# Kernel tuning notes

Measured on AMD Instinct MI355X. Metric: run time of the kernel, lower is better.

Reference implementation:

```python
import jax, jax.numpy as jnp
import numpy as np

B, L, N, F, H, ED, HOR = 64, 24, 512, 2, 128, 16, 12


def setup_inputs() -> dict:
    key = jax.random.key(0)
    ks = jax.random.split(key, 9)
    g = lambda k, shp, sc: jax.random.normal(k, shp, dtype=jnp.float32) * sc
    return {
        "X": g(ks[0], (B, L, N, F), 1.0),
        "E": g(ks[1], (N, ED), 1.0),
        "W1": g(ks[2], (ED, ED), ED ** -0.5),
        "W2": g(ks[3], (ED, ED), ED ** -0.5),
        "Wz": g(ks[4], (F + H, H), (F + H) ** -0.5),
        "bz": jnp.zeros((H,), jnp.float32),
        "Wr": g(ks[5], (F + H, H), (F + H) ** -0.5),
        "br": jnp.zeros((H,), jnp.float32),
        "Wh": g(ks[6], (F + H, H), (F + H) ** -0.5),
        "bh": jnp.zeros((H,), jnp.float32),
        "Whead": g(ks[7], (H, HOR), H ** -0.5),
        "bhead": jnp.zeros((HOR,), jnp.float32),
    }


def reference(X, E, W1, W2, Wz, bz, Wr, br, Wh, bh, Whead, bhead):
    # Adaptive adjacency: A = softmax(relu((E W1)(E W2)^T))  -> [N, N]
    M1 = E @ W1
    M2 = E @ W2
    A = jax.nn.softmax(jax.nn.relu(M1 @ M2.T), axis=-1)

    b, n, h = X.shape[0], X.shape[2], Wz.shape[1]

    def step(hprev, x_t):  # x_t: [B, N, F], hprev: [B, N, H]
        inp = jnp.concatenate([x_t, hprev], axis=-1)          # [B, N, F+H]
        g = jnp.einsum('nm,bmf->bnf', A, inp)                  # graph conv mix
        z = jax.nn.sigmoid(g @ Wz + bz)
        r = jax.nn.sigmoid(g @ Wr + br)
        inp_r = jnp.concatenate([x_t, r * hprev], axis=-1)
        gh = jnp.einsum('nm,bmf->bnf', A, inp_r)
        h_tilde = jnp.tanh(gh @ Wh + bh)
        hnew = (1.0 - z) * hprev + z * h_tilde
        return hnew, None

    h0 = jnp.zeros((b, n, h), X.dtype)
    h_final, _ = jax.lax.scan(step, h0, jnp.moveaxis(X, 1, 0))  # scan over L
    out = h_final @ Whead + bhead                                # [B, N, HOR]
    return jnp.transpose(out, (0, 2, 1))                         # [B, HOR, N]
```

## Files before the change

### kernel.cpp

```cpp
#include <hip/hip_runtime.h>

typedef _Float16 f16;
typedef _Float16 f16x8 __attribute__((ext_vector_type(8)));
typedef float f32x4 __attribute__((ext_vector_type(4)));

typedef const __attribute__((address_space(1))) void GV;
typedef __attribute__((address_space(3))) void LV;

__device__ __forceinline__ void gload16(const void* g, void* l) {
  __builtin_amdgcn_global_load_lds((GV*)g, (LV*)l, 16, 0, 0);
}

#define WAIT_VM0() asm volatile("s_waitcnt vmcnt(0)" ::: "memory")

__device__ __forceinline__ f16x8 ntload16(const f16* p) {
  f16x8 v;
  asm volatile("global_load_dwordx4 %0, %1, off sc0 sc1" : "=v"(v) : "v"(p) : "memory");
  return v;
}
__device__ __forceinline__ void ntstore16(f16* p, f16x8 v) {
  asm volatile("global_store_dwordx4 %0, %1, off sc0 sc1" :: "v"(p), "v"(v) : "memory");
}

__device__ __forceinline__ void group_sync(unsigned* bar, unsigned target) {
  __syncthreads();
  if (threadIdx.x == 0) {
    atomicAdd(bar, 1u);
    int guard = 0;
    while (1) {
      unsigned v;
      asm volatile("global_load_dword %0, %1, off sc0 sc1\n\ts_waitcnt vmcnt(0)"
                   : "=v"(v) : "v"(bar) : "memory");
      if (v >= target || ++guard > (1 << 22)) break;
      __builtin_amdgcn_s_sleep(8);
    }
  }
  __syncthreads();
}

__device__ __forceinline__ f16x8 frag64(const f16* T, int row, int chunk) {
  int ch = chunk ^ (row & 7);
  return *(const f16x8*)((const char*)T + row * 128 + ch * 16);
}
__device__ __forceinline__ f16x8 frag128(const f16* T, int row, int chunk) {
  int ch = chunk ^ (row & 15);
  return *(const f16x8*)((const char*)T + row * 256 + ch * 16);
}
__device__ __forceinline__ f16* elem128(f16* T, int row, int col) {
  return (f16*)((char*)T + row * 256 + (((col >> 3) ^ (row & 15)) << 4) + (col & 7) * 2);
}

#define MFMA(a, b, c) __builtin_amdgcn_mfma_f32_16x16x32_f16(a, b, c, 0, 0, 0)

__device__ __forceinline__ float sigm(float v) {
  return __builtin_amdgcn_rcpf(1.f + __expf(-v));
}
__device__ __forceinline__ float tanh_(float v) {
  return 1.f - 2.f * __builtin_amdgcn_rcpf(1.f + __expf(2.f * v));
}

__device__ __forceinline__ void issue64(const f16* Ab, const f16* Bb, int k0,
                                        char* bufA, f16x8 (&c)[4],
                                        const size_t (&offs)[4], int wb) {
#pragma unroll
  for (int q = 0; q < 4; ++q)
    gload16(Ab + k0 + offs[q], bufA + q * 4096 + wb);
#pragma unroll
  for (int q = 0; q < 4; ++q)
    c[q] = ntload16(Bb + k0 + offs[q]);
}
__device__ __forceinline__ void wr64(char* bufB, const f16x8 (&c)[4], int tb) {
#pragma unroll
  for (int q = 0; q < 4; ++q)
    *(f16x8*)(bufB + q * 4096 + tb) = c[q];
}
__device__ __forceinline__ void comp64(const char* buf, int wm, int wn, int g, int r,
                                       f32x4 (&acc)[4][4]) {
  const f16* Ta = (const f16*)buf;
  const f16* Tb = (const f16*)(buf + 16384);
#pragma unroll
  for (int kk = 0; kk < 2; ++kk) {
    f16x8 af[4], bf[4];
#pragma unroll
    for (int i = 0; i < 4; ++i) af[i] = frag64(Ta, wm + i * 16 + r, (kk << 2) | g);
#pragma unroll
    for (int j = 0; j < 4; ++j) bf[j] = frag64(Tb, wn + j * 16 + r, (kk << 2) | g);
#pragma unroll
    for (int i = 0; i < 4; ++i)
#pragma unroll
      for (int j = 0; j < 4; ++j)
        acc[i][j] = MFMA(af[i], bf[j], acc[i][j]);
  }
}

__device__ __forceinline__ void phase1(const f16* At, const f16* Bb, char* sm,
    const size_t (&offs)[4], int wm, int wn, int g, int r, f32x4 (&acc)[4][4]) {
  const int tid = threadIdx.x;
  const int wb = (tid >> 6) * 1024;
  const int tb = tid * 16;
  f16x8 c[4];
  issue64(At, Bb, 0, sm, c, offs, wb);
  WAIT_VM0();
  wr64(sm + 16384, c, tb);
  __syncthreads();
#pragma unroll 1
  for (int kt = 0; kt < 8; ++kt) {
    char* cur = sm + (kt & 1) * 32768;
    char* nxt = sm + ((kt & 1) ^ 1) * 32768;
    if (kt < 7) issue64(At, Bb, (kt + 1) * 64, nxt, c, offs, wb);
    comp64(cur, wm, wn, g, r, acc);
    if (kt < 7) { WAIT_VM0(); wr64(nxt + 16384, c, tb); }
    __syncthreads();
  }
}

__device__ __forceinline__ void gate_gemm(const f16* Gs, const f16* WT,
                                          int wm, int wn, int g, int r,
                                          f32x4 (&acc)[4][4]) {
#pragma unroll
  for (int kk = 0; kk < 4; ++kk) {
    f16x8 wf[4], af[4];
#pragma unroll
    for (int j = 0; j < 4; ++j)
      wf[j] = *(const f16x8*)&WT[(size_t)(wn + j * 16 + r) * 128 + kk * 32 + g * 8];
#pragma unroll
    for (int i = 0; i < 4; ++i) af[i] = frag128(Gs, wm + i * 16 + r, (kk << 2) | g);
#pragma unroll
    for (int i = 0; i < 4; ++i)
#pragma unroll
      for (int j = 0; j < 4; ++j)
        acc[i][j] = MFMA(af[i], wf[j], acc[i][j]);
  }
}

__global__ __launch_bounds__(256, 1)
void persist(const f16* __restrict__ A16, const f16* __restrict__ AX,
             const f16* __restrict__ WzT, const f16* __restrict__ WrT,
             const f16* __restrict__ WhT,
             const float* __restrict__ Wzf, const float* __restrict__ bz,
             const float* __restrict__ Wrf, const float* __restrict__ br,
             const float* __restrict__ Whf, const float* __restrict__ bh,
             const float* __restrict__ Whead, const float* __restrict__ bhead,
             f16* __restrict__ Ha, f16* __restrict__ Hb,
             f16* __restrict__ RH, unsigned* __restrict__ bar,
             float* __restrict__ out) {
  __shared__ __align__(16) char sm[136192];
  f16* Gs = (f16*)(sm + 65536);
  f16* Ct = (f16*)(sm + 98304);
  f16* AXs = (f16*)(sm + 131072);
  float* wp = (float*)(sm + 131584);

  const int tid = threadIdx.x;
  const int lane = tid & 63;
  const int g = lane >> 4, r = lane & 15;
  const int wid = tid >> 6;
  const int wm = (wid >> 1) * 64, wn = (wid & 1) * 64;
  const int b = blockIdx.x >> 2, nc = blockIdx.x & 3;
  const int m0 = nc * 128;

  for (int idx = tid; idx < 1152; idx += 256) {
    int row = idx >> 7, j = idx & 127;
    float v;
    if (row == 0) v = Wzf[j];
    else if (row == 1) v = Wzf[128 + j];
    else if (row == 2) v = bz[j];
    else if (row == 3) v = Wrf[j];
    else if (row == 4) v = Wrf[128 + j];
    else if (row == 5) v = br[j];
    else if (row == 6) v = Whf[j];
    else if (row == 7) v = Whf[128 + j];
    else v = bh[j];
    wp[idx] = v;
  }

  size_t offs[4];
#pragma unroll
  for (int q = 0; q < 4; ++q) {
    int lin = q * 4096 + tid * 16;
    int row = lin >> 7;
    int ch = ((lin >> 4) & 7) ^ (row & 7);
    offs[q] = (size_t)row * 512 + ch * 8;
  }

  const f16* Atile = A16 + (size_t)m0 * 512;
  const size_t boff = (size_t)b * 65536;
  f16* rh = RH + boff;
  unsigned* mybar = bar + b * 16;
  unsigned nbar = 0;
  f16x8 zreg[8];
  f16x8 hvreg[8] = {};

#pragma unroll 1
  for (int t = 0; t < 24; ++t) {
    const f16* hc = ((t & 1) ? Hb : Ha) + boff;
    f16* hn = ((t & 1) ? Ha : Hb) + boff;
    if (tid < 128) {
      int cf = b * 48 + t * 2;
      const f16* p = AX + (size_t)(cf >> 7) * 65536 + (size_t)(m0 + tid) * 128 + (cf & 127);
      AXs[2 * tid] = p[0];
      AXs[2 * tid + 1] = p[1];
    }
    f32x4 acc[4][4] = {};
    phase1(Atile, hc, sm, offs, wm, wn, g, r, acc);
#pragma unroll
    for (int i = 0; i < 4; ++i)
#pragma unroll
      for (int j = 0; j < 4; ++j)
#pragma unroll
        for (int q = 0; q < 4; ++q)
          *elem128(Gs, wm + i * 16 + g * 4 + q, wn + j * 16 + r) = (f16)acc[i][j][q];
    __syncthreads();
    {
      f32x4 az[4][4] = {};
      gate_gemm(Gs, WzT, wm, wn, g, r, az);
#pragma unroll
      for (int i = 0; i < 4; ++i)
#pragma unroll
        for (int j = 0; j < 4; ++j)
#pragma unroll
          for (int q = 0; q < 4; ++q)
            *elem128(Ct, wn + j * 16 + r, wm + i * 16 + g * 4 + q) = (f16)az[i][j][q];
      __syncthreads();
#pragma unroll
      for (int p = 0; p < 8; ++p) {
        int hh = p * 16 + (tid >> 4), c = tid & 15, nl0 = c * 8;
        f16x8 cv = frag128(Ct, hh, c);
        float w0 = wp[hh], w1 = wp[128 + hh], bb = wp[256 + hh];
        f16x8 o;
#pragma unroll
        for (int e = 0; e < 8; ++e) {
          int nl = nl0 + e;
          float gx = (float)AXs[2 * nl] * w0 + (float)AXs[2 * nl + 1] * w1 + bb;
          o[e] = (f16)sigm((float)cv[e] + gx);
        }
        zreg[p] = o;
      }
      __syncthreads();
    }
    {
      f32x4 ar[4][4] = {};
      gate_gemm(Gs, WrT, wm, wn, g, r, ar);
#pragma unroll
      for (int i = 0; i < 4; ++i)
#pragma unroll
        for (int j = 0; j < 4; ++j)
#pragma unroll
          for (int q = 0; q < 4; ++q)
            *elem128(Ct, wn + j * 16 + r, wm + i * 16 + g * 4 + q) = (f16)ar[i][j][q];
      __syncthreads();
#pragma unroll
      for (int p = 0; p < 8; ++p) {
        int hh = p * 16 + (tid >> 4), c = tid & 15, nl0 = c * 8;
        f16x8 cv = frag128(Ct, hh, c);
        f16x8 hv = hvreg[p];
        float w0 = wp[384 + hh], w1 = wp[512 + hh], bb = wp[640 + hh];
        f16x8 o;
#pragma unroll
        for (int e = 0; e < 8; ++e) {
          int nl = nl0 + e;
          float gx = (float)AXs[2 * nl] * w0 + (float)AXs[2 * nl + 1] * w1 + bb;
          float rv = sigm((float)cv[e] + gx);
          o[e] = (f16)(rv * (float)hv[e]);
        }
        ntstore16(&rh[(size_t)hh * 512 + m0 + nl0], o);
      }
    }
    group_sync(mybar, 4u * (++nbar));
    f32x4 acc2[4][4] = {};
    phase1(Atile, rh, sm, offs, wm, wn, g, r, acc2);
#pragma unroll
    for (int i = 0; i < 4; ++i)
#pragma unroll
      for (int j = 0; j < 4; ++j)
#pragma unroll
        for (int q = 0; q < 4; ++q)
          *elem128(Gs, wm + i * 16 + g * 4 + q, wn + j * 16 + r) = (f16)acc2[i][j][q];
    __syncthreads();
    {
      f32x4 ah[4][4] = {};
      gate_gemm(Gs, WhT, wm, wn, g, r, ah);
#pragma unroll
      for (int i = 0; i < 4; ++i)
#pragma unroll
        for (int j = 0; j < 4; ++j)
#pragma unroll
          for (int q = 0; q < 4; ++q)
            *elem128(Ct, wn + j * 16 + r, wm + i * 16 + g * 4 + q) = (f16)ah[i][j][q];
      __syncthreads();
#pragma unroll
      for (int p = 0; p < 8; ++p) {
        int hh = p * 16 + (tid >> 4), c = tid & 15, nl0 = c * 8;
        f16x8 cv = frag128(Ct, hh, c);
        float w0 = wp[768 + hh], w1 = wp[896 + hh], bb = wp[1024 + hh];
        f16x8 hv = hvreg[p], zv = zreg[p];
        f16x8 o;
#pragma unroll
        for (int e = 0; e < 8; ++e) {
          int nl = nl0 + e;
          float gx = (float)AXs[2 * nl] * w0 + (float)AXs[2 * nl + 1] * w1 + bb;
          float ht = tanh_((float)cv[e] + gx);
          float z = (float)zv[e];
          o[e] = (f16)((1.f - z) * (float)hv[e] + z * ht);
        }
        hvreg[p] = o;
        if (t < 23) {
          ntstore16(&hn[(size_t)hh * 512 + m0 + nl0], o);
        } else {
          *(f16x8*)((char*)Gs + hh * 256 + nl0 * 2) = o;
        }
      }
    }
    if (t < 23) {
      group_sync(mybar, 4u * (++nbar));
    }
  }

  __syncthreads();
  float* Ws = (float*)Ct;
  for (int idx = tid; idx < 1548; idx += 256)
    Ws[idx] = (idx < 1536) ? Whead[idx] : bhead[idx - 1536];
  __syncthreads();
  {
    int n = tid & 127, half = tid >> 7;
    float pa[12];
#pragma unroll
    for (int o = 0; o < 12; ++o) pa[o] = 0.f;
    const f16* Hfin = (const f16*)Gs;
    for (int h = half * 64; h < half * 64 + 64; ++h) {
      float v = (float)Hfin[h * 128 + n];
#pragma unroll
      for (int o = 0; o < 12; ++o) pa[o] = fmaf(v, Ws[h * 12 + o], pa[o]);
    }
    float* P = (float*)(sm + 40960);
#pragma unroll
    for (int o = 0; o < 12; ++o) P[(n * 2 + half) * 12 + o] = pa[o];
    __syncthreads();
    if (half == 0) {
#pragma unroll
      for (int o = 0; o < 12; ++o)
        out[(size_t)b * 6144 + o * 512 + m0 + n] = P[n * 24 + o] + P[n * 24 + 12 + o] + Ws[1536 + o];
    }
  }
}

__device__ __forceinline__ void stage128x64(const f16* src, int row0, int ld, int k0,
                                            f16* lds, int tid) {
  int wid = tid >> 6;
#pragma unroll
  for (int q = 0; q < 4; ++q) {
    int lin = q * 4096 + tid * 16;
    int row = lin >> 7;
    int ch = (lin >> 4) & 7;
    int sch = ch ^ (row & 7);
    gload16(src + (size_t)(row0 + row) * ld + k0 + sch * 8,
            (char*)lds + q * 4096 + wid * 1024);
  }
}

__global__ __launch_bounds__(256, 2)
void gemm512(const f16* __restrict__ A, const f16* __restrict__ B,
             f16* __restrict__ C) {
  __shared__ __align__(16) char sm[34816];
  f16* As = (f16*)sm;
  f16* Bs = (f16*)(sm + 16384);
  const int tid = threadIdx.x;
  const int lane = tid & 63;
  const int g = lane >> 4, r = lane & 15;
  const int wid = tid >> 6;
  const int wm = (wid >> 1) * 64, wn = (wid & 1) * 64;
  const int m0 = blockIdx.y * 128;
  const int n0 = blockIdx.x * 128;
  f32x4 acc[4][4] = {};
  for (int kt = 0; kt < 8; ++kt) {
    stage128x64(A, m0, 512, kt * 64, As, tid);
    stage128x64(B, n0, 512, kt * 64, Bs, tid);
    __syncthreads();
#pragma unroll
    for (int kk = 0; kk < 2; ++kk) {
      f16x8 af[4], bf[4];
#pragma unroll
      for (int i = 0; i < 4; ++i) af[i] = frag64(As, wm + i * 16 + r, (kk << 2) | g);
#pragma unroll
      for (int j = 0; j < 4; ++j) bf[j] = frag64(Bs, wn + j * 16 + r, (kk << 2) | g);
#pragma unroll
      for (int i = 0; i < 4; ++i)
#pragma unroll
        for (int j = 0; j < 4; ++j)
          acc[i][j] = MFMA(af[i], bf[j], acc[i][j]);
    }
    __syncthreads();
  }
  f16* Ctl = (f16*)sm;
#pragma unroll
  for (int i = 0; i < 4; ++i)
#pragma unroll
    for (int j = 0; j < 4; ++j) {
      int col = wn + j * 16 + r;
#pragma unroll
      for (int q = 0; q < 4; ++q) {
        int row = wm + i * 16 + g * 4 + q;
        Ctl[row * 136 + col] = (f16)acc[i][j][q];
      }
    }
  __syncthreads();
  f16* Cb = C + (size_t)blockIdx.x * 65536;
#pragma unroll
  for (int p = 0; p < 8; ++p) {
    int row = p * 16 + (tid >> 4);
    int c0 = (tid & 15) * 8;
    f16x8 v = *(const f16x8*)&Ctl[row * 136 + c0];
    *(f16x8*)&Cb[(size_t)(m0 + row) * 128 + c0] = v;
  }
}

__global__ void m12k(const float* __restrict__ E, const float* __restrict__ W1,
                     const float* __restrict__ W2, float* __restrict__ M1,
                     float* __restrict__ M2) {
  int idx = blockIdx.x * 256 + threadIdx.x;
  if (idx >= 16384) return;
  int which = idx >> 13;
  int rem = idx & 8191;
  int n = rem >> 4, j = rem & 15;
  const float* W = which ? W2 : W1;
  float s = 0.f;
#pragma unroll
  for (int k = 0; k < 16; ++k) s += E[n * 16 + k] * W[k * 16 + j];
  (which ? M2 : M1)[n * 16 + j] = s;
}

__global__ __launch_bounds__(256)
void softA(const float* __restrict__ M1, const float* __restrict__ M2,
           f16* __restrict__ A16) {
  __shared__ float M2s[8192];
  __shared__ float m1s[16];
  __shared__ float red[8];
  int i = blockIdx.x, tid = threadIdx.x;
  for (int q = tid; q < 8192; q += 256) M2s[q] = M2[q];
  if (tid < 16) m1s[tid] = M1[i * 16 + tid];
  __syncthreads();
  float s0 = 0.f, s1 = 0.f;
#pragma unroll
  for (int k = 0; k < 16; ++k) {
    float a = m1s[k];
    s0 += a * M2s[tid * 16 + k];
    s1 += a * M2s[(tid + 256) * 16 + k];
  }
  s0 = fmaxf(s0, 0.f);
  s1 = fmaxf(s1, 0.f);
  float m = fmaxf(s0, s1);
  for (int o = 32; o > 0; o >>= 1) m = fmaxf(m, __shfl_xor(m, o));
  if ((tid & 63) == 0) red[tid >> 6] = m;
  __syncthreads();
  m = fmaxf(fmaxf(red[0], red[1]), fmaxf(red[2], red[3]));
  float e0 = expf(s0 - m), e1 = expf(s1 - m);
  float ss = e0 + e1;
  for (int o = 32; o > 0; o >>= 1) ss += __shfl_xor(ss, o);
  __syncthreads();
  if ((tid & 63) == 0) red[4 + (tid >> 6)] = ss;
  __syncthreads();
  ss = (red[4] + red[5]) + (red[6] + red[7]);
  float inv = 1.f / ss;
  A16[(size_t)i * 512 + tid] = (f16)(e0 * inv);
  A16[(size_t)i * 512 + tid + 256] = (f16)(e1 * inv);
}

__global__ void wTk(const float* __restrict__ Wz, const float* __restrict__ Wr,
                    const float* __restrict__ Wh, f16* __restrict__ WzT,
                    f16* __restrict__ WrT, f16* __restrict__ WhT) {
  int idx = blockIdx.x * 256 + threadIdx.x;
  if (idx >= 49152) return;
  int w = idx / 16384;
  int rem = idx & 16383;
  int hp = rem >> 7, k = rem & 127;
  const float* S = (w == 0) ? Wz : ((w == 1) ? Wr : Wh);
  f16* D = (w == 0) ? WzT : ((w == 1) ? WrT : WhT);
  D[hp * 128 + k] = (f16)S[(2 + k) * 128 + hp];
}

__global__ void xTk(const float* __restrict__ X, f16* __restrict__ XTT) {
  int idx = blockIdx.x * 256 + threadIdx.x;
  if (idx >= 786432) return;
  int m = idx & 511;
  int bt = idx >> 9;
  float x0 = X[(size_t)idx * 2];
  float x1 = X[(size_t)idx * 2 + 1];
  XTT[(size_t)(bt * 2 + 0) * 512 + m] = (f16)x0;
  XTT[(size_t)(bt * 2 + 1) * 512 + m] = (f16)x1;
}

extern "C" void kernel_launch(void* const* d_in, const int* in_sizes, int n_in,
                              void* d_out, int out_size, void* d_ws, size_t ws_size,
                              hipStream_t stream) {
  (void)in_sizes; (void)n_in; (void)out_size; (void)ws_size;
  const float* X = (const float*)d_in[0];
  const float* E = (const float*)d_in[1];
  const float* W1 = (const float*)d_in[2];
  const float* W2 = (const float*)d_in[3];
  const float* Wz = (const float*)d_in[4];
  const float* bz = (const float*)d_in[5];
  const float* Wr = (const float*)d_in[6];
  const float* br = (const float*)d_in[7];
  const float* Wh = (const float*)d_in[8];
  const float* bh = (const float*)d_in[9];
  const float* Whead = (const float*)d_in[10];
  const float* bhead = (const float*)d_in[11];
  float* out = (float*)d_out;
  char* ws = (char*)d_ws;

  f16* A16 = (f16*)(ws + 0);
  f16* XTT = (f16*)(ws + 524288);
  f16* AX  = (f16*)(ws + 3670016);
  f16* Ha  = (f16*)(ws + 6815744);
  f16* Hb  = (f16*)(ws + 15204352);
  f16* RH  = (f16*)(ws + 23592960);
  f16* WzT = (f16*)(ws + 31981568);
  f16* WrT = (f16*)(ws + 32014336);
  f16* WhT = (f16*)(ws + 32047104);
  float* M1 = (float*)(ws + 32079872);
  float* M2 = (float*)(ws + 32112640);
  unsigned* bar = (unsigned*)(ws + 32145408);

  hipMemsetAsync(Ha, 0, 8388608, stream);
  hipMemsetAsync(bar, 0, 16384, stream);
  m12k<<<64, 256, 0, stream>>>(E, W1, W2, M1, M2);
  softA<<<512, 256, 0, stream>>>(M1, M2, A16);
  wTk<<<192, 256, 0, stream>>>(Wz, Wr, Wh, WzT, WrT, WhT);
  xTk<<<3072, 256, 0, stream>>>(X, XTT);
  gemm512<<<dim3(24, 4), 256, 0, stream>>>(A16, XTT, AX);
  persist<<<256, 256, 0, stream>>>(A16, AX, WzT, WrT, WhT, Wz, bz, Wr, br, Wh, bh,
                                   Whead, bhead, Ha, Hb, RH, bar, out);
}
```

Measured before the change: 796.3 us.

## Merge two node-chunk blocks into one 512-thread block per half-batch

The persistent GRU kernel now runs 128 blocks of 512 threads instead of 256 blocks of 256. Each 256-thread half handles its own 128-node chunk with a private LDS region, and the scratch buffers now overlap the phase-1 double buffer. Only two blocks per batch join the cross-block group barrier, so the barrier target is halved, and an explicit vmcnt wait is added before each barrier. The cost is that only half as many CUs are used, block-wide __syncthreads now couples both halves, and launch bounds of (512,2) may tighten the register budget.

```diff
diff --git a/kernel.cpp b/kernel.cpp
--- a/kernel.cpp
+++ b/kernel.cpp
@@ -93,20 +93,20 @@
   }
 }
 
-__device__ __forceinline__ void phase1(const f16* At, const f16* Bb, char* sm,
-    const size_t (&offs)[4], int wm, int wn, int g, int r, f32x4 (&acc)[4][4]) {
-  const int tid = threadIdx.x;
-  const int wb = (tid >> 6) * 1024;
-  const int tb = tid * 16;
+__device__ __forceinline__ void phase1(const f16* At, const f16* Bb, char* base,
+    const size_t (&offs)[4], int ltid, int wm, int wn, int g, int r,
+    f32x4 (&acc)[4][4]) {
+  const int wb = (ltid >> 6) * 1024;
+  const int tb = ltid * 16;
   f16x8 c[4];
-  issue64(At, Bb, 0, sm, c, offs, wb);
+  issue64(At, Bb, 0, base, c, offs, wb);
   WAIT_VM0();
-  wr64(sm + 16384, c, tb);
+  wr64(base + 16384, c, tb);
   __syncthreads();
 #pragma unroll 1
   for (int kt = 0; kt < 8; ++kt) {
-    char* cur = sm + (kt & 1) * 32768;
-    char* nxt = sm + ((kt & 1) ^ 1) * 32768;
+    char* cur = base + (kt & 1) * 32768;
+    char* nxt = base + ((kt & 1) ^ 1) * 32768;
     if (kt < 7) issue64(At, Bb, (kt + 1) * 64, nxt, c, offs, wb);
     comp64(cur, wm, wn, g, r, acc);
     if (kt < 7) { WAIT_VM0(); wr64(nxt + 16384, c, tb); }
@@ -133,7 +133,7 @@
   }
 }
 
-__global__ __launch_bounds__(256, 1)
+__global__ __launch_bounds__(512, 2)
 void persist(const f16* __restrict__ A16, const f16* __restrict__ AX,
              const f16* __restrict__ WzT, const f16* __restrict__ WrT,
              const f16* __restrict__ WhT,
@@ -144,21 +144,26 @@
              f16* __restrict__ Ha, f16* __restrict__ Hb,
              f16* __restrict__ RH, unsigned* __restrict__ bar,
              float* __restrict__ out) {
-  __shared__ __align__(16) char sm[136192];
-  f16* Gs = (f16*)(sm + 65536);
-  f16* Ct = (f16*)(sm + 98304);
-  f16* AXs = (f16*)(sm + 131072);
-  float* wp = (float*)(sm + 131584);
+  __shared__ __align__(16) char sm[136704];
 
   const int tid = threadIdx.x;
-  const int lane = tid & 63;
+  const int e = tid >> 8;
+  const int ltid = tid & 255;
+  const int lane = ltid & 63;
   const int g = lane >> 4, r = lane & 15;
-  const int wid = tid >> 6;
-  const int wm = (wid >> 1) * 64, wn = (wid & 1) * 64;
-  const int b = blockIdx.x >> 2, nc = blockIdx.x & 3;
+  const int wid4 = (ltid >> 6) & 3;
+  const int wm = (wid4 >> 1) * 64, wn = (wid4 & 1) * 64;
+  const int b = blockIdx.x >> 1, half = blockIdx.x & 1;
+  const int nc = half * 2 + e;
   const int m0 = nc * 128;
 
-  for (int idx = tid; idx < 1152; idx += 256) {
+  char* eng = sm + e * 65536;
+  f16* Gs = (f16*)(eng + 32768);
+  f16* Ct = (f16*)(eng + 0);
+  f16* AXs = (f16*)(sm + 131072) + e * 256;
+  float* wp = (float*)(sm + 132096);
+
+  for (int idx = tid; idx < 1152; idx += 512) {
     int row = idx >> 7, j = idx & 127;
     float v;
     if (row == 0) v = Wzf[j];
@@ -176,7 +181,7 @@
   size_t offs[4];
 #pragma unroll
   for (int q = 0; q < 4; ++q) {
-    int lin = q * 4096 + tid * 16;
+    int lin = q * 4096 + ltid * 16;
     int row = lin >> 7;
     int ch = ((lin >> 4) & 7) ^ (row & 7);
     offs[q] = (size_t)row * 512 + ch * 8;
@@ -189,19 +194,20 @@
   unsigned nbar = 0;
   f16x8 zreg[8];
   f16x8 hvreg[8] = {};
+  __syncthreads();
 
 #pragma unroll 1
   for (int t = 0; t < 24; ++t) {
     const f16* hc = ((t & 1) ? Hb : Ha) + boff;
     f16* hn = ((t & 1) ? Ha : Hb) + boff;
-    if (tid < 128) {
+    if (ltid < 128) {
       int cf = b * 48 + t * 2;
-      const f16* p = AX + (size_t)(cf >> 7) * 65536 + (size_t)(m0 + tid) * 128 + (cf & 127);
-      AXs[2 * tid] = p[0];
-      AXs[2 * tid + 1] = p[1];
+      const f16* p = AX + (size_t)(cf >> 7) * 65536 + (size_t)(m0 + ltid) * 128 + (cf & 127);
+      AXs[2 * ltid] = p[0];
+      AXs[2 * ltid + 1] = p[1];
     }
     f32x4 acc[4][4] = {};
-    phase1(Atile, hc, sm, offs, wm, wn, g, r, acc);
+    phase1(Atile, hc, eng, offs, ltid, wm, wn, g, r, acc);
 #pragma unroll
     for (int i = 0; i < 4; ++i)
 #pragma unroll
@@ -223,15 +229,15 @@
       __syncthreads();
 #pragma unroll
       for (int p = 0; p < 8; ++p) {
-        int hh = p * 16 + (tid >> 4), c = tid & 15, nl0 = c * 8;
+        int hh = p * 16 + (ltid >> 4), c = ltid & 15, nl0 = c * 8;
         f16x8 cv = frag128(Ct, hh, c);
         float w0 = wp[hh], w1 = wp[128 + hh], bb = wp[256 + hh];
         f16x8 o;
 #pragma unroll
-        for (int e = 0; e < 8; ++e) {
-          int nl = nl0 + e;
+        for (int u = 0; u < 8; ++u) {
+          int nl = nl0 + u;
           float gx = (float)AXs[2 * nl] * w0 + (float)AXs[2 * nl + 1] * w1 + bb;
-          o[e] = (f16)sigm((float)cv[e] + gx);
+          o[u] = (f16)sigm((float)cv[u] + gx);
         }
         zreg[p] = o;
       }
@@ -250,24 +256,25 @@
       __syncthreads();
 #pragma unroll
       for (int p = 0; p < 8; ++p) {
-        int hh = p * 16 + (tid >> 4), c = tid & 15, nl0 = c * 8;
+        int hh = p * 16 + (ltid >> 4), c = ltid & 15, nl0 = c * 8;
         f16x8 cv = frag128(Ct, hh, c);
         f16x8 hv = hvreg[p];
         float w0 = wp[384 + hh], w1 = wp[512 + hh], bb = wp[640 + hh];
         f16x8 o;
 #pragma unroll
-        for (int e = 0; e < 8; ++e) {
-          int nl = nl0 + e;
+        for (int u = 0; u < 8; ++u) {
+          int nl = nl0 + u;
           float gx = (float)AXs[2 * nl] * w0 + (float)AXs[2 * nl + 1] * w1 + bb;
-          float rv = sigm((float)cv[e] + gx);
-          o[e] = (f16)(rv * (float)hv[e]);
+          float rv = sigm((float)cv[u] + gx);
+          o[u] = (f16)(rv * (float)hv[u]);
         }
         ntstore16(&rh[(size_t)hh * 512 + m0 + nl0], o);
       }
-    }
-    group_sync(mybar, 4u * (++nbar));
+      WAIT_VM0();
+    }
+    group_sync(mybar, 2u * (++nbar));
     f32x4 acc2[4][4] = {};
-    phase1(Atile, rh, sm, offs, wm, wn, g, r, acc2);
+    phase1(Atile, rh, eng, offs, ltid, wm, wn, g, r, acc2);
 #pragma unroll
     for (int i = 0; i < 4; ++i)
 #pragma unroll
@@ -289,18 +296,18 @@
       __syncthreads();
 #pragma unroll
       for (int p = 0; p < 8; ++p) {
-        int hh = p * 16 + (tid >> 4), c = tid & 15, nl0 = c * 8;
+        int hh = p * 16 + (ltid >> 4), c = ltid & 15, nl0 = c * 8;
         f16x8 cv = frag128(Ct, hh, c);
         float w0 = wp[768 + hh], w1 = wp[896 + hh], bb = wp[1024 + hh];
         f16x8 hv = hvreg[p], zv = zreg[p];
         f16x8 o;
 #pragma unroll
-        for (int e = 0; e < 8; ++e) {
-          int nl = nl0 + e;
+        for (int u = 0; u < 8; ++u) {
+          int nl = nl0 + u;
           float gx = (float)AXs[2 * nl] * w0 + (float)AXs[2 * nl + 1] * w1 + bb;
-          float ht = tanh_((float)cv[e] + gx);
-          float z = (float)zv[e];
-          o[e] = (f16)((1.f - z) * (float)hv[e] + z * ht);
+          float ht = tanh_((float)cv[u] + gx);
+          float z = (float)zv[u];
+          o[u] = (f16)((1.f - z) * (float)hv[u] + z * ht);
         }
         hvreg[p] = o;
         if (t < 23) {
@@ -309,36 +316,38 @@
           *(f16x8*)((char*)Gs + hh * 256 + nl0 * 2) = o;
         }
       }
+      if (t < 23) WAIT_VM0();
     }
     if (t < 23) {
-      group_sync(mybar, 4u * (++nbar));
+      group_sync(mybar, 2u * (++nbar));
     }
   }
 
   __syncthreads();
   float* Ws = (float*)Ct;
-  for (int idx = tid; idx < 1548; idx += 256)
+  for (int idx = ltid; idx < 1548; idx += 256)
     Ws[idx] = (idx < 1536) ? Whead[idx] : bhead[idx - 1536];
   __syncthreads();
   {
-    int n = tid & 127, half = tid >> 7;
+    int n = ltid & 127, hf = ltid >> 7;
     float pa[12];
 #pragma unroll
     for (int o = 0; o < 12; ++o) pa[o] = 0.f;
     const f16* Hfin = (const f16*)Gs;
-    for (int h = half * 64; h < half * 64 + 64; ++h) {
+    for (int h = hf * 64; h < hf * 64 + 64; ++h) {
       float v = (float)Hfin[h * 128 + n];
 #pragma unroll
       for (int o = 0; o < 12; ++o) pa[o] = fmaf(v, Ws[h * 12 + o], pa[o]);
     }
-    float* P = (float*)(sm + 40960);
-#pragma unroll
-    for (int o = 0; o < 12; ++o) P[(n * 2 + half) * 12 + o] = pa[o];
+    float* P = (float*)(eng + 16384);
+#pragma unroll
+    for (int o = 0; o < 12; ++o) P[(n * 2 + hf) * 12 + o] = pa[o];
     __syncthreads();
-    if (half == 0) {
+    if (hf == 0) {
 #pragma unroll
       for (int o = 0; o < 12; ++o)
-        out[(size_t)b * 6144 + o * 512 + m0 + n] = P[n * 24 + o] + P[n * 24 + 12 + o] + Ws[1536 + o];
+        out[(size_t)b * 6144 + o * 512 + m0 + n] =
+            P[n * 24 + o] + P[n * 24 + 12 + o] + Ws[1536 + o];
     }
   }
 }
@@ -527,6 +536,6 @@
   wTk<<<192, 256, 0, stream>>>(Wz, Wr, Wh, WzT, WrT, WhT);
   xTk<<<3072, 256, 0, stream>>>(X, XTT);
   gemm512<<<dim3(24, 4), 256, 0, stream>>>(A16, XTT, AX);
-  persist<<<256, 256, 0, stream>>>(A16, AX, WzT, WrT, WhT, Wz, bz, Wr, br, Wh, bh,
+  persist<<<128, 512, 0, stream>>>(A16, AX, WzT, WrT, WhT, Wz, bz, Wr, br, Wh, bh,
                                    Whead, bhead, Ha, Hb, RH, bar, out);
 }
```

Result: slower. 1.820 ms (+128.6%).
